# Performance work log

Measured on AMD Instinct MI355X. Metric: run time of the kernel, lower is better.

The kernel has to match this reference:

```python
import jax, jax.numpy as jnp
import numpy as np

H, KVH, D = 32, 8, 128
HID = H * D
OP = H * D + 2 * KVH * D
T = 2048
LAYER_IDX = 8
LAMBDA_INIT = float(0.8 - 0.6 * np.exp(-0.3 * LAYER_IDX))
EPS = 1e-5


def setup_inputs() -> dict:
    key = jax.random.key(0)
    ks = jax.random.split(key, 10)
    s = 0.02
    return {
        "hidden_states": jax.random.normal(ks[0], (T, HID), jnp.float32),
        "wqkv_w": jax.random.normal(ks[1], (OP, HID), jnp.float32) * s,
        "wqkv_b": jax.random.normal(ks[2], (OP,), jnp.float32) * s,
        "lambda_q1": jax.random.normal(ks[3], (D,), jnp.float32) * 0.1,
        "lambda_k1": jax.random.normal(ks[4], (D,), jnp.float32) * 0.1,
        "lambda_q2": jax.random.normal(ks[5], (D,), jnp.float32) * 0.1,
        "lambda_k2": jax.random.normal(ks[6], (D,), jnp.float32) * 0.1,
        "subln_w": jnp.ones((2 * D,), jnp.float32),
        "out_w": jax.random.normal(ks[7], (HID, HID), jnp.float32) * s,
        "out_b": jax.random.normal(ks[8], (HID,), jnp.float32) * s,
    }


def reference(hidden_states, wqkv_w, wqkv_b, lambda_q1, lambda_k1,
              lambda_q2, lambda_k2, subln_w, out_w, out_b):
    t = hidden_states.shape[0]
    scale = D ** -0.5

    qkv = hidden_states @ wqkv_w.T + wqkv_b                     # [T, OP]
    q, k, v = jnp.split(qkv, [H * D, H * D + KVH * D], axis=-1)

    # pair-wise head split: consecutive heads form (pair, component) groups
    q = q.reshape(t, H // 2, 2, D)                              # [T, Hp, 2, D]
    k = k.reshape(t, KVH // 2, 2, D)                            # [T, KVHp, 2, D]
    v = v.reshape(t, KVH // 2, 2 * D)                           # [T, KVHp, 2D]

    rep = H // KVH  # GQA: query pair p -> kv pair p // rep
    k = jnp.repeat(k, rep, axis=1)                              # [T, Hp, 2, D]
    v = jnp.repeat(v, rep, axis=1)                              # [T, Hp, 2D]

    lam = (jnp.exp(jnp.dot(lambda_q1, lambda_k1))
           - jnp.exp(jnp.dot(lambda_q2, lambda_k2)) + LAMBDA_INIT)

    causal = jnp.tril(jnp.ones((t, t), bool))
    scores = jnp.einsum('qhcd,khcd->hcqk', q, k) * scale        # [Hp, 2, T, T]
    scores = jnp.where(causal, scores, -jnp.inf)
    probs = jax.nn.softmax(scores, axis=-1)
    attn = probs[:, 0] - lam * probs[:, 1]                      # [Hp, T, T]

    out = jnp.einsum('hqk,khd->qhd', attn, v)                   # [T, Hp, 2D]

    # per-head RMSNorm over 2D, scaled by (1 - lambda_init)
    rms = jax.lax.rsqrt(jnp.mean(out * out, axis=-1, keepdims=True) + EPS)
    out = out * rms * subln_w * (1.0 - LAMBDA_INIT)

    out = out.reshape(t, H * D)
    return out @ out_w.T + out_b
```

## Files before the change

kernel.cpp:

```cpp
#include <hip/hip_runtime.h>

#define TTOK 2048
#define HIDN 4096
#define OPD  6144
#define DH   128
#define VD   256
#define KOFF 4096
#define VOFF 5120

typedef short  s16x8 __attribute__((ext_vector_type(8)));
typedef unsigned short u16x8 __attribute__((ext_vector_type(8)));
typedef float  fx4   __attribute__((ext_vector_type(4)));

constexpr float LAM_INIT = 0.7455692280263534f;
constexpr float OML      = 1.0f - LAM_INIT;
constexpr float QKSCALE  = 0.08838834764831845f;
constexpr float RESCALE_THR = 8.0f;

__device__ __forceinline__ unsigned short f2bf(float f) {
  unsigned int u = __builtin_bit_cast(unsigned int, f);
  u += 0x7fffu + ((u >> 16) & 1u);
  return (unsigned short)(u >> 16);
}

__device__ __forceinline__ void g2l16(const void* gsrc, void* ldst) {
  __builtin_amdgcn_global_load_lds(
      (const __attribute__((address_space(1))) unsigned int*)gsrc,
      (__attribute__((address_space(3))) unsigned int*)ldst, 16, 0, 0);
}

__global__ __launch_bounds__(256)
void cvt3(const float* __restrict__ s0, unsigned short* __restrict__ d0, int nb0,
          const float* __restrict__ s1, unsigned short* __restrict__ d1, int nb1,
          const float* __restrict__ s2, unsigned short* __restrict__ d2)
{
  const int b = blockIdx.x;
  const float* s; unsigned short* d; int base;
  if (b < nb0)            { s = s0; d = d0; base = b << 11; }
  else if (b < nb0 + nb1) { s = s1; d = d1; base = (b - nb0) << 11; }
  else                    { s = s2; d = d2; base = (b - nb0 - nb1) << 11; }
  const int i = base + (int)threadIdx.x * 8;
  const float4 a0 = *(const float4*)(s + i);
  const float4 a1 = *(const float4*)(s + i + 4);
  u16x8 v;
  v[0]=f2bf(a0.x); v[1]=f2bf(a0.y); v[2]=f2bf(a0.z); v[3]=f2bf(a0.w);
  v[4]=f2bf(a1.x); v[5]=f2bf(a1.y); v[6]=f2bf(a1.z); v[7]=f2bf(a1.w);
  *(u16x8*)(d + i) = v;
}

__global__ __launch_bounds__(256)
void reduce2(const float* __restrict__ p, const float* __restrict__ bias,
             float* __restrict__ out)
{
  const size_t i = ((size_t)blockIdx.x * 256 + threadIdx.x) * 4;
  const int col = (int)(i & (HIDN - 1));
  const float4 a = *(const float4*)(p + i);
  const float4 b = *(const float4*)(p + (size_t)TTOK * HIDN + i);
  const float4 c = *(const float4*)(bias + col);
  float4 r;
  r.x = a.x + b.x + c.x; r.y = a.y + b.y + c.y;
  r.z = a.z + b.z + c.z; r.w = a.w + b.w + c.w;
  *(float4*)(out + i) = r;
}

__global__ __launch_bounds__(512, 2)
void gemm1_qkv(const unsigned short* __restrict__ A, const unsigned short* __restrict__ B,
               const float* __restrict__ bias, unsigned short* __restrict__ qq,
               unsigned short* __restrict__ ctt)
{
  __shared__ __align__(16) unsigned short As[2][2][128 * 64];
  __shared__ __align__(16) unsigned short Bs[2][192 * 64];

  const int tid  = threadIdx.x;
  const int lane = tid & 63, wid = tid >> 6;
  const int wm = wid >> 1, wn = wid & 1;
  const int m0 = blockIdx.y * 256, n0 = blockIdx.x * 192;
  const int l15 = lane & 15, lg = lane >> 4;

  const int scol = ((tid & 7) ^ ((tid >> 3) & 7)) << 3;
  const int rsw = (l15 & 7) << 3;
  const int ck0 = (lg * 8) ^ rsw;
  const int ck1 = (32 + lg * 8) ^ rsw;
  const int arh = wm * 16 + l15;
  const int brh = wn * 96 + l15;

  auto stageAh = [&](int kt, int buf, int h) {
    #pragma unroll
    for (int i = 0; i < 2; ++i) {
      const int li = i * 512 + tid;
      g2l16(A + (size_t)(m0 + h * 128 + (li >> 3)) * HIDN + kt + scol,
            &As[buf][h][li * 8]);
    }
  };
  auto stageB = [&](int kt, int buf) {
    #pragma unroll
    for (int i = 0; i < 3; ++i) {
      const int li = i * 512 + tid;
      g2l16(B + (size_t)(n0 + (li >> 3)) * HIDN + kt + scol,
            &Bs[buf][li * 8]);
    }
  };

  fx4 acc[4][6] = {};

  const int nk = HIDN >> 6;
  stageAh(0, 0, 0); stageB(0, 0); stageAh(0, 0, 1);
  asm volatile("s_waitcnt vmcnt(0)" ::: "memory");
  __builtin_amdgcn_s_barrier();

  for (int t = 0; t < nk; ++t) {
    const int buf = t & 1, nb = buf ^ 1;
    const int kt1 = (t + 1) << 6;
    const bool pre = (t + 1) < nk;
    const unsigned short* A0 = &As[buf][0][0];
    const unsigned short* A1 = &As[buf][1][0];
    const unsigned short* Bp = &Bs[buf][0];
    s16x8 af[2], bk0[6], bk1[6];

    af[0] = *(const s16x8*)&A0[(arh)      * 64 + ck0];
    af[1] = *(const s16x8*)&A0[(arh + 64) * 64 + ck0];
    #pragma unroll
    for (int n = 0; n < 6; ++n)
      bk0[n] = *(const s16x8*)&Bp[(brh + n * 16) * 64 + ck0];
    if (pre) {
      stageAh(kt1, nb, 0);
      asm volatile("s_waitcnt vmcnt(2)" ::: "memory");
    } else {
      asm volatile("s_waitcnt vmcnt(0)" ::: "memory");
    }
    __builtin_amdgcn_s_barrier();
    __builtin_amdgcn_s_setprio(1);
    #pragma unroll
    for (int m = 0; m < 2; ++m)
      #pragma unroll
      for (int n = 0; n < 6; ++n)
        acc[m][n] = __builtin_amdgcn_mfma_f32_16x16x32_bf16(af[m], bk0[n], acc[m][n], 0, 0, 0);
    __builtin_amdgcn_s_setprio(0);

    af[0] = *(const s16x8*)&A0[(arh)      * 64 + ck1];
    af[1] = *(const s16x8*)&A0[(arh + 64) * 64 + ck1];
    #pragma unroll
    for (int n = 0; n < 6; ++n)
      bk1[n] = *(const s16x8*)&Bp[(brh + n * 16) * 64 + ck1];
    if (pre) stageB(kt1, nb);
    __builtin_amdgcn_s_barrier();
    __builtin_amdgcn_s_setprio(1);
    #pragma unroll
    for (int m = 0; m < 2; ++m)
      #pragma unroll
      for (int n = 0; n < 6; ++n)
        acc[m][n] = __builtin_amdgcn_mfma_f32_16x16x32_bf16(af[m], bk1[n], acc[m][n], 0, 0, 0);
    __builtin_amdgcn_s_setprio(0);

    af[0] = *(const s16x8*)&A1[(arh)      * 64 + ck0];
    af[1] = *(const s16x8*)&A1[(arh + 64) * 64 + ck0];
    if (pre) stageAh(kt1, nb, 1);
    __builtin_amdgcn_s_setprio(1);
    #pragma unroll
    for (int m = 0; m < 2; ++m)
      #pragma unroll
      for (int n = 0; n < 6; ++n)
        acc[2 + m][n] = __builtin_amdgcn_mfma_f32_16x16x32_bf16(af[m], bk0[n], acc[2 + m][n], 0, 0, 0);
    __builtin_amdgcn_s_setprio(0);

    af[0] = *(const s16x8*)&A1[(arh)      * 64 + ck1];
    af[1] = *(const s16x8*)&A1[(arh + 64) * 64 + ck1];
    __builtin_amdgcn_s_setprio(1);
    #pragma unroll
    for (int m = 0; m < 2; ++m)
      #pragma unroll
      for (int n = 0; n < 6; ++n)
        acc[2 + m][n] = __builtin_amdgcn_mfma_f32_16x16x32_bf16(af[m], bk1[n], acc[2 + m][n], 0, 0, 0);
    __builtin_amdgcn_s_setprio(0);
  }

  #pragma unroll
  for (int mi = 0; mi < 4; ++mi)
    #pragma unroll
    for (int ni = 0; ni < 6; ++ni) {
      const int colg = n0 + wn * 96 + ni * 16;
      const int col  = colg + l15;
      const float bv = bias[col];
      const fx4 a = acc[mi][ni];
      const int row0 = m0 + mi * 64 + wm * 16 + lg * 4;
      if (colg >= VOFF) {
        ushort4 pk;
        pk.x = f2bf(a[0] + bv); pk.y = f2bf(a[1] + bv);
        pk.z = f2bf(a[2] + bv); pk.w = f2bf(a[3] + bv);
        const int d = col - VOFF;
        const int kvp = d >> 8, dw = d & 255;
        const int kt2 = row0 >> 5, kk = row0 & 31;
        const int kc = kk >> 3, k8 = kk & 7;
        *(ushort4*)&ctt[(size_t)kvp * 1048576 + (size_t)kt2 * 16384 + 8192
                        + kc * 2048 + dw * 8 + k8] = pk;
      } else if (colg >= KOFF) {
        const int ccol = col - KOFF;
        const int kvp = ccol >> 8, cw = ccol & 255;
        const int cc = cw >> 3, cbt = cw & 7;
        #pragma unroll
        for (int jj = 0; jj < 4; ++jj) {
          const int row2 = row0 + jj;
          const int kt2 = row2 >> 5, kk = row2 & 31;
          ctt[(size_t)kvp * 1048576 + (size_t)kt2 * 16384 + cc * 256 + kk * 8 + cbt]
              = f2bf(a[jj] + bv);
        }
      } else {
        #pragma unroll
        for (int jj = 0; jj < 4; ++jj)
          qq[(size_t)(row0 + jj) * HIDN + col] = f2bf((a[jj] + bv) * QKSCALE);
      }
    }
}

__global__ __launch_bounds__(512, 2)
void gemm2_sk(const unsigned short* __restrict__ A, const unsigned short* __restrict__ B,
              float* __restrict__ P, int K, int lda, int ldb, int ldc)
{
  __shared__ __align__(16) unsigned short As[2][2][128 * 64];
  __shared__ __align__(16) unsigned short Bs[2][2][128 * 64];

  const int tid  = threadIdx.x;
  const int lane = tid & 63, wid = tid >> 6;
  const int wm = wid >> 2, wn = wid & 3;
  const int m0 = blockIdx.y * 256, n0 = blockIdx.x * 256;
  const int l15 = lane & 15, lg = lane >> 4;
  const int kOff = blockIdx.z * K;

  const int scol = ((tid & 7) ^ ((tid >> 3) & 7)) << 3;
  const int rsw = (l15 & 7) << 3;
  const int ck0 = (lg * 8) ^ rsw;
  const int ck1 = (32 + lg * 8) ^ rsw;
  const int arh = wm * 16 + l15;
  const int brh = wn * 16 + l15;

  auto stageAh = [&](int kt, int buf, int h) {
    #pragma unroll
    for (int i = 0; i < 2; ++i) {
      const int li = i * 512 + tid;
      g2l16(A + (size_t)(m0 + h * 128 + (li >> 3)) * lda + kOff + kt + scol,
            &As[buf][h][li * 8]);
    }
  };
  auto stageBh = [&](int kt, int buf, int h) {
    #pragma unroll
    for (int i = 0; i < 2; ++i) {
      const int li = i * 512 + tid;
      g2l16(B + (size_t)(n0 + h * 128 + (li >> 3)) * ldb + kOff + kt + scol,
            &Bs[buf][h][li * 8]);
    }
  };

  fx4 acc[8][4] = {};

  const int nk = K >> 6;
  stageAh(0, 0, 0); stageBh(0, 0, 0); stageBh(0, 0, 1); stageAh(0, 0, 1);
  asm volatile("s_waitcnt vmcnt(0)" ::: "memory");
  __builtin_amdgcn_s_barrier();

  for (int t = 0; t < nk; ++t) {
    const int buf = t & 1, nb = buf ^ 1;
    const int kt1 = (t + 1) << 6;
    const bool pre = (t + 1) < nk;
    const unsigned short* A0 = &As[buf][0][0];
    const unsigned short* A1 = &As[buf][1][0];
    const unsigned short* B0 = &Bs[buf][0][0];
    const unsigned short* B1 = &Bs[buf][1][0];
    s16x8 af[4][2], bf0[2][2], bf1[2][2];

    #pragma unroll
    for (int m = 0; m < 4; ++m) {
      af[m][0] = *(const s16x8*)&A0[(arh + m * 32) * 64 + ck0];
      af[m][1] = *(const s16x8*)&A0[(arh + m * 32) * 64 + ck1];
    }
    #pragma unroll
    for (int n = 0; n < 2; ++n) {
      bf0[n][0] = *(const s16x8*)&B0[(brh + n * 64) * 64 + ck0];
      bf0[n][1] = *(const s16x8*)&B0[(brh + n * 64) * 64 + ck1];
    }
    if (pre) {
      stageAh(kt1, nb, 0);
      asm volatile("s_waitcnt vmcnt(4)" ::: "memory");
    } else {
      asm volatile("s_waitcnt vmcnt(0)" ::: "memory");
    }
    __builtin_amdgcn_s_barrier();
    __builtin_amdgcn_s_setprio(1);
    #pragma unroll
    for (int m = 0; m < 4; ++m)
      #pragma unroll
      for (int n = 0; n < 2; ++n) {
        acc[m][n] = __builtin_amdgcn_mfma_f32_16x16x32_bf16(af[m][0], bf0[n][0], acc[m][n], 0, 0, 0);
        acc[m][n] = __builtin_amdgcn_mfma_f32_16x16x32_bf16(af[m][1], bf0[n][1], acc[m][n], 0, 0, 0);
      }
    __builtin_amdgcn_s_setprio(0);

    #pragma unroll
    for (int n = 0; n < 2; ++n) {
      bf1[n][0] = *(const s16x8*)&B1[(brh + n * 64) * 64 + ck0];
      bf1[n][1] = *(const s16x8*)&B1[(brh + n * 64) * 64 + ck1];
    }
    if (pre) {
      stageBh(kt1, nb, 0);
      asm volatile("s_waitcnt vmcnt(4)" ::: "memory");
    }
    __builtin_amdgcn_s_barrier();
    __builtin_amdgcn_s_setprio(1);
    #pragma unroll
    for (int m = 0; m < 4; ++m)
      #pragma unroll
      for (int n = 0; n < 2; ++n) {
        acc[m][2 + n] = __builtin_amdgcn_mfma_f32_16x16x32_bf16(af[m][0], bf1[n][0], acc[m][2 + n], 0, 0, 0);
        acc[m][2 + n] = __builtin_amdgcn_mfma_f32_16x16x32_bf16(af[m][1], bf1[n][1], acc[m][2 + n], 0, 0, 0);
      }
    __builtin_amdgcn_s_setprio(0);

    #pragma unroll
    for (int m = 0; m < 4; ++m) {
      af[m][0] = *(const s16x8*)&A1[(arh + m * 32) * 64 + ck0];
      af[m][1] = *(const s16x8*)&A1[(arh + m * 32) * 64 + ck1];
    }
    if (pre) stageBh(kt1, nb, 1);
    __builtin_amdgcn_s_setprio(1);
    #pragma unroll
    for (int m = 0; m < 4; ++m)
      #pragma unroll
      for (int n = 0; n < 2; ++n) {
        acc[4 + m][2 + n] = __builtin_amdgcn_mfma_f32_16x16x32_bf16(af[m][0], bf1[n][0], acc[4 + m][2 + n], 0, 0, 0);
        acc[4 + m][2 + n] = __builtin_amdgcn_mfma_f32_16x16x32_bf16(af[m][1], bf1[n][1], acc[4 + m][2 + n], 0, 0, 0);
      }
    __builtin_amdgcn_s_setprio(0);

    if (pre) stageAh(kt1, nb, 1);
    __builtin_amdgcn_s_setprio(1);
    #pragma unroll
    for (int m = 0; m < 4; ++m)
      #pragma unroll
      for (int n = 0; n < 2; ++n) {
        acc[4 + m][n] = __builtin_amdgcn_mfma_f32_16x16x32_bf16(af[m][0], bf0[n][0], acc[4 + m][n], 0, 0, 0);
        acc[4 + m][n] = __builtin_amdgcn_mfma_f32_16x16x32_bf16(af[m][1], bf0[n][1], acc[4 + m][n], 0, 0, 0);
      }
    __builtin_amdgcn_s_setprio(0);
    if (pre) asm volatile("s_waitcnt vmcnt(4)" ::: "memory");
    __builtin_amdgcn_s_barrier();
  }

  float* Pz = P + (size_t)blockIdx.z * TTOK * ldc;
  const int rb = m0 + wm * 16;
  const int cb = n0 + wn * 16;
  #pragma unroll
  for (int mi = 0; mi < 8; ++mi)
    #pragma unroll
    for (int ni = 0; ni < 4; ++ni) {
      const int col = cb + ni * 64 + l15;
      const fx4 a = acc[mi][ni];
      #pragma unroll
      for (int jj = 0; jj < 4; ++jj)
        Pz[(size_t)(rb + mi * 32 + lg * 4 + jj) * ldc + col] = a[jj];
    }
}

__global__ __launch_bounds__(256, 2)
void attn_kernel(const unsigned short* __restrict__ qq,
                 const unsigned short* __restrict__ ctt,
                 const float* __restrict__ lq1, const float* __restrict__ lk1,
                 const float* __restrict__ lq2, const float* __restrict__ lk2,
                 const float* __restrict__ subln,
                 unsigned short* __restrict__ attn_out)
{
  __shared__ __align__(16) unsigned short Sb[2][16384];
  __shared__ __align__(16) unsigned short Pl[4][2][640];
  const int tid = threadIdx.x;
  const int lane = tid & 63, w = tid >> 6;
  const int l15 = lane & 15, lg = lane >> 4;

  const int bid  = blockIdx.x;
  const int r    = bid & 255;
  const int pair = r & 15;
  const int x    = r >> 4;
  const int qb   = (bid >> 8) ? x : 31 - x;
  const int kvp  = pair >> 2;
  const int q0b  = qb * 64;
  const int q0w  = q0b + w * 16;
  const int nt   = 2 * qb + 2;

  const unsigned short* cbase = ctt + (size_t)kvp * 1048576;

  auto stage = [&](int kt, int buf) {
    const unsigned short* src = cbase + (size_t)kt * 16384;
    const int off = w * 512 + lane * 8;
    #pragma unroll
    for (int i = 0; i < 8; ++i) {
      const int o = i * 2048 + off;
      g2l16(src + o, &Sb[buf][o]);
    }
  };

  stage(0, 0);

  float a1 = lq1[lane] * lk1[lane] + lq1[lane + 64] * lk1[lane + 64];
  float a2 = lq2[lane] * lk2[lane] + lq2[lane + 64] * lk2[lane + 64];
  #pragma unroll
  for (int sft = 1; sft < 64; sft <<= 1) { a1 += __shfl_xor(a1, sft); a2 += __shfl_xor(a2, sft); }
  const float lam = __expf(a1) - __expf(a2) + LAM_INIT;

  s16x8 qf0[4], qf1[4];
  {
    const unsigned short* qbp = qq + (size_t)(q0w + l15) * HIDN + pair * VD + lg * 8;
    #pragma unroll
    for (int kf = 0; kf < 4; ++kf) {
      qf0[kf] = *(const s16x8*)(qbp + kf * 32);
      qf1[kf] = *(const s16x8*)(qbp + DH + kf * 32);
    }
  }

  float mrun0 = -1e30f, mrun1 = -1e30f;
  float lrun0 = 0.f, lrun1 = 0.f;
  fx4 oacc0[16] = {}, oacc1[16] = {};
  unsigned short* pl0 = &Pl[w][0][0];
  unsigned short* pl1 = &Pl[w][1][0];
  const int q = q0w + l15;
  const int qmax = q0w + 15;

  for (int t = 0; t < nt; ++t) {
    __syncthreads();
    if (t + 1 < nt) stage(t + 1, (t + 1) & 1);
    const int kb = t * 32;
    if (kb > qmax) continue;
    const unsigned short* Kl = Sb[t & 1];
    const unsigned short* Vl = Sb[t & 1] + 8192;

    fx4 s00 = {0,0,0,0}, s01 = {0,0,0,0}, s10 = {0,0,0,0}, s11 = {0,0,0,0};
    #pragma unroll
    for (int kf = 0; kf < 4; ++kf) {
      const int cc0 = kf * 4 + lg;
      const int cc1 = 16 + kf * 4 + lg;
      const s16x8 k00 = *(const s16x8*)&Kl[cc0 * 256 + l15 * 8];
      const s16x8 k01 = *(const s16x8*)&Kl[cc0 * 256 + (16 + l15) * 8];
      const s16x8 k10 = *(const s16x8*)&Kl[cc1 * 256 + l15 * 8];
      const s16x8 k11 = *(const s16x8*)&Kl[cc1 * 256 + (16 + l15) * 8];
      s00 = __builtin_amdgcn_mfma_f32_16x16x32_bf16(k00, qf0[kf], s00, 0, 0, 0);
      s01 = __builtin_amdgcn_mfma_f32_16x16x32_bf16(k01, qf0[kf], s01, 0, 0, 0);
      s10 = __builtin_amdgcn_mfma_f32_16x16x32_bf16(k10, qf1[kf], s10, 0, 0, 0);
      s11 = __builtin_amdgcn_mfma_f32_16x16x32_bf16(k11, qf1[kf], s11, 0, 0, 0);
    }

    float v0[8], v1[8];
    if (kb + 32 <= q0w) {
      #pragma unroll
      for (int j = 0; j < 4; ++j) {
        v0[j] = s00[j]; v0[4 + j] = s01[j];
        v1[j] = s10[j]; v1[4 + j] = s11[j];
      }
    } else {
      #pragma unroll
      for (int j = 0; j < 4; ++j) {
        const int klo = kb + lg * 4 + j, khi = klo + 16;
        v0[j]     = (klo <= q) ? s00[j] : -1e30f;
        v0[4 + j] = (khi <= q) ? s01[j] : -1e30f;
        v1[j]     = (klo <= q) ? s10[j] : -1e30f;
        v1[4 + j] = (khi <= q) ? s11[j] : -1e30f;
      }
    }
    float tm0 = fmaxf(fmaxf(fmaxf(v0[0],v0[1]),fmaxf(v0[2],v0[3])),
                      fmaxf(fmaxf(v0[4],v0[5]),fmaxf(v0[6],v0[7])));
    float tm1 = fmaxf(fmaxf(fmaxf(v1[0],v1[1]),fmaxf(v1[2],v1[3])),
                      fmaxf(fmaxf(v1[4],v1[5]),fmaxf(v1[6],v1[7])));
    tm0 = fmaxf(tm0, __shfl_xor(tm0, 16)); tm0 = fmaxf(tm0, __shfl_xor(tm0, 32));
    tm1 = fmaxf(tm1, __shfl_xor(tm1, 16)); tm1 = fmaxf(tm1, __shfl_xor(tm1, 32));

    const bool need = (tm0 > mrun0 + RESCALE_THR) || (tm1 > mrun1 + RESCALE_THR);
    if (__any(need)) {
      const float mn0 = fmaxf(mrun0, tm0), mn1 = fmaxf(mrun1, tm1);
      const float fac0 = __expf(mrun0 - mn0), fac1 = __expf(mrun1 - mn1);
      mrun0 = mn0; mrun1 = mn1;
      lrun0 *= fac0; lrun1 *= fac1;
      #pragma unroll
      for (int jj = 0; jj < 4; ++jj) {
        const float fr0 = __shfl(fac0, lg * 4 + jj);
        const float fr1 = __shfl(fac1, lg * 4 + jj);
        #pragma unroll
        for (int nf = 0; nf < 16; ++nf) { oacc0[nf][jj] *= fr0; oacc1[nf][jj] *= fr1; }
      }
    }

    {
      float ps0 = 0.f, ps1 = 0.f;
      ushort4 lo0, hi0, lo1, hi1;
      float p;
      p = __expf(v0[0]-mrun0); ps0 += p; lo0.x = f2bf(p);
      p = __expf(v0[1]-mrun0); ps0 += p; lo0.y = f2bf(p);
      p = __expf(v0[2]-mrun0); ps0 += p; lo0.z = f2bf(p);
      p = __expf(v0[3]-mrun0); ps0 += p; lo0.w = f2bf(p);
      p = __expf(v0[4]-mrun0); ps0 += p; hi0.x = f2bf(p);
      p = __expf(v0[5]-mrun0); ps0 += p; hi0.y = f2bf(p);
      p = __expf(v0[6]-mrun0); ps0 += p; hi0.z = f2bf(p);
      p = __expf(v0[7]-mrun0); ps0 += p; hi0.w = f2bf(p);
      p = __expf(v1[0]-mrun1); ps1 += p; lo1.x = f2bf(p);
      p = __expf(v1[1]-mrun1); ps1 += p; lo1.y = f2bf(p);
      p = __expf(v1[2]-mrun1); ps1 += p; lo1.z = f2bf(p);
      p = __expf(v1[3]-mrun1); ps1 += p; lo1.w = f2bf(p);
      p = __expf(v1[4]-mrun1); ps1 += p; hi1.x = f2bf(p);
      p = __expf(v1[5]-mrun1); ps1 += p; hi1.y = f2bf(p);
      p = __expf(v1[6]-mrun1); ps1 += p; hi1.z = f2bf(p);
      p = __expf(v1[7]-mrun1); ps1 += p; hi1.w = f2bf(p);
      lrun0 += ps0; lrun1 += ps1;
      *(ushort4*)&pl0[l15 * 40 + lg * 4]      = lo0;
      *(ushort4*)&pl0[l15 * 40 + 16 + lg * 4] = hi0;
      *(ushort4*)&pl1[l15 * 40 + lg * 4]      = lo1;
      *(ushort4*)&pl1[l15 * 40 + 16 + lg * 4] = hi1;
    }
    asm volatile("s_waitcnt lgkmcnt(0)" ::: "memory");
    __builtin_amdgcn_sched_barrier(0);

    const s16x8 pa0 = *(const s16x8*)&pl0[l15 * 40 + lg * 8];
    const s16x8 pa1 = *(const s16x8*)&pl1[l15 * 40 + lg * 8];
    #pragma unroll
    for (int nf = 0; nf < 16; ++nf) {
      const s16x8 vf = *(const s16x8*)&Vl[lg * 2048 + (nf * 16 + l15) * 8];
      oacc0[nf] = __builtin_amdgcn_mfma_f32_16x16x32_bf16(pa0, vf, oacc0[nf], 0, 0, 0);
      oacc1[nf] = __builtin_amdgcn_mfma_f32_16x16x32_bf16(pa1, vf, oacc1[nf], 0, 0, 0);
    }
  }

  lrun0 += __shfl_xor(lrun0, 16); lrun0 += __shfl_xor(lrun0, 32);
  lrun1 += __shfl_xor(lrun1, 16); lrun1 += __shfl_xor(lrun1, 32);

  float li0[4], li1[4];
  #pragma unroll
  for (int jj = 0; jj < 4; ++jj) {
    li0[jj] = 1.0f / __shfl(lrun0, lg * 4 + jj);
    li1[jj] = 1.0f / __shfl(lrun1, lg * 4 + jj);
  }

  float ss[4] = {0.f, 0.f, 0.f, 0.f};
  #pragma unroll
  for (int nf = 0; nf < 16; ++nf)
    #pragma unroll
    for (int jj = 0; jj < 4; ++jj) {
      const float o = oacc0[nf][jj] * li0[jj] - lam * oacc1[nf][jj] * li1[jj];
      oacc0[nf][jj] = o;
      ss[jj] += o * o;
    }
  #pragma unroll
  for (int jj = 0; jj < 4; ++jj) {
    ss[jj] += __shfl_xor(ss[jj], 1);
    ss[jj] += __shfl_xor(ss[jj], 2);
    ss[jj] += __shfl_xor(ss[jj], 4);
    ss[jj] += __shfl_xor(ss[jj], 8);
    ss[jj] = rsqrtf(ss[jj] * (1.0f / 256.0f) + 1e-5f) * OML;
  }
  #pragma unroll
  for (int nf = 0; nf < 16; ++nf) {
    const int dcol = nf * 16 + l15;
    const float sw = subln[dcol];
    #pragma unroll
    for (int jj = 0; jj < 4; ++jj) {
      const int t = q0w + lg * 4 + jj;
      attn_out[(size_t)t * HIDN + pair * VD + dcol] = f2bf(oacc0[nf][jj] * ss[jj] * sw);
    }
  }
}

extern "C" void kernel_launch(void* const* d_in, const int* in_sizes, int n_in,
                              void* d_out, int out_size, void* d_ws, size_t ws_size,
                              hipStream_t stream) {
  (void)in_sizes; (void)n_in; (void)out_size; (void)ws_size;
  const float* hs     = (const float*)d_in[0];
  const float* wqkv_w = (const float*)d_in[1];
  const float* wqkv_b = (const float*)d_in[2];
  const float* lq1    = (const float*)d_in[3];
  const float* lk1    = (const float*)d_in[4];
  const float* lq2    = (const float*)d_in[5];
  const float* lk2    = (const float*)d_in[6];
  const float* subln  = (const float*)d_in[7];
  const float* out_w  = (const float*)d_in[8];
  const float* out_b  = (const float*)d_in[9];

  unsigned short* qq       = (unsigned short*)d_ws;
  unsigned short* ctt      = qq + (size_t)TTOK * HIDN;
  unsigned short* attn_out = ctt + (size_t)4 * 1048576;
  unsigned short* hs_bf    = attn_out + (size_t)TTOK * HIDN;
  unsigned short* wqkv_bf  = hs_bf + (size_t)TTOK * HIDN;
  unsigned short* outw_bf  = wqkv_bf + (size_t)OPD * HIDN;
  float*          partial  = (float*)hs_bf;

  const int nb0 = (TTOK * HIDN) >> 11;
  const int nb1 = (OPD * HIDN) >> 11;
  const int nb2 = (HIDN * HIDN) >> 11;
  cvt3<<<dim3(nb0 + nb1 + nb2), 256, 0, stream>>>(
      hs, hs_bf, nb0, wqkv_w, wqkv_bf, nb1, out_w, outw_bf);

  gemm1_qkv<<<dim3(OPD / 192, TTOK / 256), 512, 0, stream>>>(
      hs_bf, wqkv_bf, wqkv_b, qq, ctt);

  attn_kernel<<<dim3(512), 256, 0, stream>>>(
      qq, ctt, lq1, lk1, lq2, lk2, subln, attn_out);

  gemm2_sk<<<dim3(HIDN / 256, TTOK / 256, 2), 512, 0, stream>>>(
      attn_out, outw_bf, partial, HIDN / 2, HIDN, HIDN, HIDN);

  reduce2<<<dim3((TTOK * HIDN) / 1024), 256, 0, stream>>>(
      partial, out_b, (float*)d_out);
}
```

Before: 331.1 us.

## Load K/V fragments directly from global memory instead of LDS double-buffering

Removes the shared-memory double-buffered K/V staging and block-wide barriers in the attention kernel. Each wave now reads K and V fragments straight from global memory (relying on L1/L2) and runs only the tiles its own 16 queries need, so causal work is no longer tied to the block's slowest wave. The launch-bounds occupancy hint is dropped. In exchange, K/V reuse across the four waves goes through cache instead of LDS, and global-load latency lands directly on the MFMA path.

```diff
diff --git a/kernel.cpp b/kernel.cpp
--- a/kernel.cpp
+++ b/kernel.cpp
@@ -359,7 +359,7 @@
     }
 }
 
-__global__ __launch_bounds__(256, 2)
+__global__ __launch_bounds__(256)
 void attn_kernel(const unsigned short* __restrict__ qq,
                  const unsigned short* __restrict__ ctt,
                  const float* __restrict__ lq1, const float* __restrict__ lk1,
@@ -367,7 +367,6 @@
                  const float* __restrict__ subln,
                  unsigned short* __restrict__ attn_out)
 {
-  __shared__ __align__(16) unsigned short Sb[2][16384];
   __shared__ __align__(16) unsigned short Pl[4][2][640];
   const int tid = threadIdx.x;
   const int lane = tid & 63, w = tid >> 6;
@@ -381,21 +380,8 @@
   const int kvp  = pair >> 2;
   const int q0b  = qb * 64;
   const int q0w  = q0b + w * 16;
-  const int nt   = 2 * qb + 2;
 
   const unsigned short* cbase = ctt + (size_t)kvp * 1048576;
-
-  auto stage = [&](int kt, int buf) {
-    const unsigned short* src = cbase + (size_t)kt * 16384;
-    const int off = w * 512 + lane * 8;
-    #pragma unroll
-    for (int i = 0; i < 8; ++i) {
-      const int o = i * 2048 + off;
-      g2l16(src + o, &Sb[buf][o]);
-    }
-  };
-
-  stage(0, 0);
 
   float a1 = lq1[lane] * lk1[lane] + lq1[lane + 64] * lk1[lane + 64];
   float a2 = lq2[lane] * lk2[lane] + lq2[lane + 64] * lk2[lane + 64];
@@ -419,25 +405,22 @@
   unsigned short* pl0 = &Pl[w][0][0];
   unsigned short* pl1 = &Pl[w][1][0];
   const int q = q0w + l15;
-  const int qmax = q0w + 15;
-
-  for (int t = 0; t < nt; ++t) {
-    __syncthreads();
-    if (t + 1 < nt) stage(t + 1, (t + 1) & 1);
+  const int ntw = q0w / 32 + 1;
+
+  for (int t = 0; t < ntw; ++t) {
     const int kb = t * 32;
-    if (kb > qmax) continue;
-    const unsigned short* Kl = Sb[t & 1];
-    const unsigned short* Vl = Sb[t & 1] + 8192;
+    const unsigned short* Kt = cbase + (size_t)t * 16384;
+    const unsigned short* Vt = Kt + 8192;
 
     fx4 s00 = {0,0,0,0}, s01 = {0,0,0,0}, s10 = {0,0,0,0}, s11 = {0,0,0,0};
     #pragma unroll
     for (int kf = 0; kf < 4; ++kf) {
       const int cc0 = kf * 4 + lg;
       const int cc1 = 16 + kf * 4 + lg;
-      const s16x8 k00 = *(const s16x8*)&Kl[cc0 * 256 + l15 * 8];
-      const s16x8 k01 = *(const s16x8*)&Kl[cc0 * 256 + (16 + l15) * 8];
-      const s16x8 k10 = *(const s16x8*)&Kl[cc1 * 256 + l15 * 8];
-      const s16x8 k11 = *(const s16x8*)&Kl[cc1 * 256 + (16 + l15) * 8];
+      const s16x8 k00 = *(const s16x8*)&Kt[cc0 * 256 + l15 * 8];
+      const s16x8 k01 = *(const s16x8*)&Kt[cc0 * 256 + (16 + l15) * 8];
+      const s16x8 k10 = *(const s16x8*)&Kt[cc1 * 256 + l15 * 8];
+      const s16x8 k11 = *(const s16x8*)&Kt[cc1 * 256 + (16 + l15) * 8];
       s00 = __builtin_amdgcn_mfma_f32_16x16x32_bf16(k00, qf0[kf], s00, 0, 0, 0);
       s01 = __builtin_amdgcn_mfma_f32_16x16x32_bf16(k01, qf0[kf], s01, 0, 0, 0);
       s10 = __builtin_amdgcn_mfma_f32_16x16x32_bf16(k10, qf1[kf], s10, 0, 0, 0);
@@ -516,7 +499,7 @@
     const s16x8 pa1 = *(const s16x8*)&pl1[l15 * 40 + lg * 8];
     #pragma unroll
     for (int nf = 0; nf < 16; ++nf) {
-      const s16x8 vf = *(const s16x8*)&Vl[lg * 2048 + (nf * 16 + l15) * 8];
+      const s16x8 vf = *(const s16x8*)&Vt[lg * 2048 + (nf * 16 + l15) * 8];
       oacc0[nf] = __builtin_amdgcn_mfma_f32_16x16x32_bf16(pa0, vf, oacc0[nf], 0, 0, 0);
       oacc1[nf] = __builtin_amdgcn_mfma_f32_16x16x32_bf16(pa1, vf, oacc1[nf], 0, 0, 0);
     }
```

New measurement: 470.2 us. 1.42x slower.
